# Kernel tuning notes

Hardware: AMD Instinct MI355X
Metric: run time of the kernel (lower is better)

The kernel has to match this reference:

```python
import jax, jax.numpy as jnp
import numpy as np

H = 2048       # hidden_size
E = 8          # num_experts
K = 2          # top_k
I = 16         # expert bottleneck (intermediate_size)


def setup_inputs() -> dict:
    key = jax.random.key(0)
    k1, k2, k3, k4 = jax.random.split(key, 4)
    B, T = 2, 4096
    x = jax.random.normal(k1, (B, T, H), dtype=jnp.float32)
    # nn.Linear weight layout is (out, in); init scale ~ 1/sqrt(fan_in)
    router_w = jax.random.normal(k2, (E, H), dtype=jnp.float32) / np.sqrt(H)
    down_w = jax.random.normal(k3, (E, I, H), dtype=jnp.float32) / np.sqrt(H)
    up_w = jax.random.normal(k4, (E, H, I), dtype=jnp.float32) / np.sqrt(I)
    return {"x": x, "router_w": router_w, "down_w": down_w, "up_w": up_w}


def reference(x, router_w, down_w, up_w):
    # router
    logits = jnp.einsum('bth,eh->bte', x, router_w)        # [B,T,E]
    weights = jax.nn.softmax(logits, axis=-1)
    top_w, top_idx = jax.lax.top_k(weights, K)             # [B,T,K]
    # gate[b,t,e] = softmax weight if e in top-k else 0 (top-k of softmax
    # values are distinct a.s., so masking == scatter of top_w)
    topk_mask = jnp.sum(jax.nn.one_hot(top_idx, E, dtype=x.dtype), axis=-2)  # [B,T,E]
    gate = weights * topk_mask                              # [B,T,E]
    # dense expert compute on all tokens (matches original's redundant compute)
    h = jnp.einsum('bth,eih->beti', x, down_w)             # [B,E,T,I]
    a = jax.nn.silu(h)
    expert_out = jnp.einsum('beti,ehi->beth', a, up_w)     # [B,E,T,H]
    # masked combine
    out = jnp.einsum('beth,bte->bth', expert_out, gate)    # [B,T,H]
    return out
```

## Files before the change

kernel.cpp:

```cpp
#include <hip/hip_runtime.h>
#include <math.h>

#define HDIM 2048
#define NEXP 8
#define IDIM 16
#define N_EI 128
#define TB   16

typedef __attribute__((ext_vector_type(8))) short bf16x8;
typedef __attribute__((ext_vector_type(4))) float f32x4;

static __device__ __forceinline__ short f2bf(float f) {
    union { float f; unsigned u; } v; v.f = f;
    unsigned r = v.u + 0x7fffu + ((v.u >> 16) & 1u);
    return (short)(r >> 16);
}

__global__ __launch_bounds__(256) void prep_kernel(
    const float* __restrict__ x, const float* __restrict__ rw,
    const float* __restrict__ dw, const float* __restrict__ uw,
    float* __restrict__ gate_ws, short* __restrict__ b1p, short* __restrict__ b2p,
    int T, int routerBlocks)
{
    const int bid = blockIdx.x;
    if (bid < routerBlocks) {
        const int wave = threadIdx.x >> 6, lane = threadIdx.x & 63;
        const int t = bid * 4 + wave;
        if (t >= T) return;
        const float* __restrict__ xr = x + (size_t)t * HDIM;
        float4 xv[8];
        #pragma unroll
        for (int j = 0; j < 8; ++j) xv[j] = *(const float4*)(xr + j * 256 + lane * 4);
        float logit[NEXP];
        #pragma unroll
        for (int e = 0; e < NEXP; ++e) {
            const float* __restrict__ wr = rw + (size_t)e * HDIM;
            float acc = 0.f;
            #pragma unroll
            for (int j = 0; j < 8; ++j) {
                float4 wv = *(const float4*)(wr + j * 256 + lane * 4);
                acc += xv[j].x * wv.x + xv[j].y * wv.y + xv[j].z * wv.z + xv[j].w * wv.w;
            }
            #pragma unroll
            for (int s = 1; s < 64; s <<= 1) acc += __shfl_xor(acc, s);
            logit[e] = acc;
        }
        if (lane == 0) {
            float m = logit[0];
            #pragma unroll
            for (int e = 1; e < NEXP; ++e) m = fmaxf(m, logit[e]);
            float w[NEXP], ssum = 0.f;
            #pragma unroll
            for (int e = 0; e < NEXP; ++e) { w[e] = expf(logit[e] - m); ssum += w[e]; }
            const float inv = 1.f / ssum;
            #pragma unroll
            for (int e = 0; e < NEXP; ++e) w[e] *= inv;
            int i1 = 0; float w1 = w[0];
            #pragma unroll
            for (int e = 1; e < NEXP; ++e) if (w[e] > w1) { w1 = w[e]; i1 = e; }
            int i2 = -1; float w2 = -1.f;
            #pragma unroll
            for (int e = 0; e < NEXP; ++e) if (e != i1 && w[e] > w2) { w2 = w[e]; i2 = e; }
            #pragma unroll
            for (int e = 0; e < NEXP; ++e)
                gate_ws[(size_t)t * NEXP + e] = (e == i1) ? w1 : ((e == i2) ? w2 : 0.f);
        }
    } else {
        const int id = (bid - routerBlocks) * 256 + threadIdx.x;
        float4 v0, v1;
        short* dst;
        if (id < 32768) {
            const int kb = id >> 7, n = id & 127;
            const float* __restrict__ src = dw + (size_t)n * HDIM + kb * 8;
            v0 = *(const float4*)(src);
            v1 = *(const float4*)(src + 4);
            dst = b1p + (size_t)id * 8;
        } else {
            const int id2 = id - 32768;
            const int k2b = id2 >> 11, h = id2 & 2047;
            const int e = k2b >> 1, i0 = (k2b & 1) * 8;
            const float* __restrict__ src = uw + ((size_t)e * HDIM + h) * IDIM + i0;
            v0 = *(const float4*)(src);
            v1 = *(const float4*)(src + 4);
            dst = b2p + (size_t)id2 * 8;
        }
        bf16x8 p;
        p[0] = f2bf(v0.x); p[1] = f2bf(v0.y); p[2] = f2bf(v0.z); p[3] = f2bf(v0.w);
        p[4] = f2bf(v1.x); p[5] = f2bf(v1.y); p[6] = f2bf(v1.z); p[7] = f2bf(v1.w);
        *(bf16x8*)dst = p;
    }
}

__global__ __launch_bounds__(512) void moe_mfma_kernel(
    const float* __restrict__ x, const float* __restrict__ gate_ws,
    const short* __restrict__ b1p, const short* __restrict__ b2p,
    float* __restrict__ out, int T)
{
    __shared__ float h_part[TB][132];
    __shared__ short a_s[TB][136];
    __shared__ float gate_s[TB][NEXP];

    const int tid = threadIdx.x;
    const int w = tid >> 6, l = tid & 63;
    const int c = l & 15;
    const int kblk = l >> 4;
    const int t0 = blockIdx.x * TB;

    if (tid < TB * NEXP)
        gate_s[tid >> 3][tid & 7] = gate_ws[(size_t)(t0 + (tid >> 3)) * NEXP + (tid & 7)];
    __syncthreads();

    const int nq = w & 3, kh = w >> 2;
    const int n0 = nq * 32;
    f32x4 acc0 = {0.f, 0.f, 0.f, 0.f}, acc1 = {0.f, 0.f, 0.f, 0.f};
    const float* __restrict__ xrow = x + (size_t)(t0 + c) * HDIM;

    for (int s = 0; s < 32; ++s) {
        const int k0 = kh * 1024 + s * 32;
        const int ka = k0 + kblk * 8;
        float4 a0 = *(const float4*)(xrow + ka);
        float4 a1 = *(const float4*)(xrow + ka + 4);
        bf16x8 xf;
        xf[0] = f2bf(a0.x); xf[1] = f2bf(a0.y); xf[2] = f2bf(a0.z); xf[3] = f2bf(a0.w);
        xf[4] = f2bf(a1.x); xf[5] = f2bf(a1.y); xf[6] = f2bf(a1.z); xf[7] = f2bf(a1.w);
        const short* __restrict__ bbase = b1p + ((size_t)(k0 >> 3) + kblk) * 1024;
        bf16x8 wf0 = *(const bf16x8*)(bbase + (n0 + c) * 8);
        bf16x8 wf1 = *(const bf16x8*)(bbase + (n0 + 16 + c) * 8);
        acc0 = __builtin_amdgcn_mfma_f32_16x16x32_bf16(wf0, xf, acc0, 0, 0, 0);
        acc1 = __builtin_amdgcn_mfma_f32_16x16x32_bf16(wf1, xf, acc1, 0, 0, 0);
    }

    if (kh == 1) {
        *(f32x4*)&h_part[c][n0 + kblk * 4]      = acc0;
        *(f32x4*)&h_part[c][n0 + 16 + kblk * 4] = acc1;
    }
    __syncthreads();
    if (kh == 0) {
        const int e0 = nq * 2, e1 = nq * 2 + 1;
        const f32x4 hp0 = *(const f32x4*)&h_part[c][n0 + kblk * 4];
        const f32x4 hp1 = *(const f32x4*)&h_part[c][n0 + 16 + kblk * 4];
        const float g0 = gate_s[c][e0], g1 = gate_s[c][e1];
        short r0[4], r1[4];
        #pragma unroll
        for (int r = 0; r < 4; ++r) {
            const float h0v = acc0[r] + hp0[r];
            const float h1v = acc1[r] + hp1[r];
            r0[r] = f2bf(h0v / (1.f + expf(-h0v)) * g0);
            r1[r] = f2bf(h1v / (1.f + expf(-h1v)) * g1);
        }
        *(uint2*)&a_s[c][n0 + kblk * 4]      = make_uint2(((unsigned short)r0[0]) | ((unsigned)(unsigned short)r0[1] << 16),
                                                          ((unsigned short)r0[2]) | ((unsigned)(unsigned short)r0[3] << 16));
        *(uint2*)&a_s[c][n0 + 16 + kblk * 4] = make_uint2(((unsigned short)r1[0]) | ((unsigned)(unsigned short)r1[1] << 16),
                                                          ((unsigned short)r1[2]) | ((unsigned)(unsigned short)r1[3] << 16));
    }
    __syncthreads();

    const int h0 = w * 256;
    f32x4 acc[16];
    #pragma unroll
    for (int f = 0; f < 16; ++f) acc[f] = (f32x4){0.f, 0.f, 0.f, 0.f};

    for (int s = 0; s < 4; ++s) {
        bf16x8 af = *(const bf16x8*)(&a_s[c][s * 32 + kblk * 8]);
        const short* __restrict__ bbase = b2p + ((size_t)(s * 4) + kblk) * 16384;
        #pragma unroll
        for (int f = 0; f < 16; ++f) {
            bf16x8 wfr = *(const bf16x8*)(bbase + (size_t)(h0 + f * 16 + c) * 8);
            acc[f] = __builtin_amdgcn_mfma_f32_16x16x32_bf16(wfr, af, acc[f], 0, 0, 0);
        }
    }
    float* __restrict__ orow = out + (size_t)(t0 + c) * HDIM;
    #pragma unroll
    for (int f = 0; f < 16; ++f) {
        __builtin_nontemporal_store(acc[f], (f32x4*)(orow + h0 + f * 16 + kblk * 4));
    }
}

extern "C" void kernel_launch(void* const* d_in, const int* in_sizes, int n_in,
                              void* d_out, int out_size, void* d_ws, size_t ws_size,
                              hipStream_t stream) {
    const float* x  = (const float*)d_in[0];
    const float* rw = (const float*)d_in[1];
    const float* dw = (const float*)d_in[2];
    const float* uw = (const float*)d_in[3];
    float* out = (float*)d_out;
    const int T = in_sizes[0] / HDIM;

    float* gate_ws = (float*)d_ws;
    short* b1p = (short*)((char*)d_ws + (size_t)T * NEXP * 4);
    short* b2p = (short*)((char*)d_ws + (size_t)T * NEXP * 4 + 524288);

    const int routerBlocks = T / 4;
    prep_kernel<<<routerBlocks + 256, 256, 0, stream>>>(x, rw, dw, uw,
                                                        gate_ws, b1p, b2p, T, routerBlocks);
    moe_mfma_kernel<<<T / TB, 512, 0, stream>>>(x, gate_ws, b1p, b2p, out, T);
}
```

Baseline: 180.4 us.

## Double token tile, pre-convert x to bf16, batch router shuffle reductions

Raises the token tile per block from 16 to 32, so each loaded weight fragment feeds two MFMAs in both the down and up projections, which halves weight traffic per token. When the workspace is large enough, the prep kernel also writes a bf16 copy of x so the main kernel reads half the bytes and skips per-element conversion, at the cost of an extra full pass over x. The router's cross-lane reductions are interleaved across all experts for more instruction-level parallelism. Output stores switch from nontemporal to normal stores, and the doubled accumulators raise register pressure with half as many blocks.

Result: faster. 172.5 us (-4.4%).

```diff
diff --git a/kernel.cpp b/kernel.cpp
--- a/kernel.cpp
+++ b/kernel.cpp
@@ -5,7 +5,7 @@
 #define NEXP 8
 #define IDIM 16
 #define N_EI 128
-#define TB   16
+#define TB   32
 
 typedef __attribute__((ext_vector_type(8))) short bf16x8;
 typedef __attribute__((ext_vector_type(4))) float f32x4;
@@ -20,18 +20,17 @@
     const float* __restrict__ x, const float* __restrict__ rw,
     const float* __restrict__ dw, const float* __restrict__ uw,
     float* __restrict__ gate_ws, short* __restrict__ b1p, short* __restrict__ b2p,
-    int T, int routerBlocks)
+    short* __restrict__ x_bf, int T, int routerBlocks)
 {
     const int bid = blockIdx.x;
     if (bid < routerBlocks) {
         const int wave = threadIdx.x >> 6, lane = threadIdx.x & 63;
         const int t = bid * 4 + wave;
-        if (t >= T) return;
         const float* __restrict__ xr = x + (size_t)t * HDIM;
         float4 xv[8];
         #pragma unroll
         for (int j = 0; j < 8; ++j) xv[j] = *(const float4*)(xr + j * 256 + lane * 4);
-        float logit[NEXP];
+        float accv[NEXP];
         #pragma unroll
         for (int e = 0; e < NEXP; ++e) {
             const float* __restrict__ wr = rw + (size_t)e * HDIM;
@@ -41,17 +40,20 @@
                 float4 wv = *(const float4*)(wr + j * 256 + lane * 4);
                 acc += xv[j].x * wv.x + xv[j].y * wv.y + xv[j].z * wv.z + xv[j].w * wv.w;
             }
-            #pragma unroll
-            for (int s = 1; s < 64; s <<= 1) acc += __shfl_xor(acc, s);
-            logit[e] = acc;
+            accv[e] = acc;
+        }
+        #pragma unroll
+        for (int s = 1; s < 64; s <<= 1) {
+            #pragma unroll
+            for (int e = 0; e < NEXP; ++e) accv[e] += __shfl_xor(accv[e], s);
         }
         if (lane == 0) {
-            float m = logit[0];
-            #pragma unroll
-            for (int e = 1; e < NEXP; ++e) m = fmaxf(m, logit[e]);
+            float m = accv[0];
+            #pragma unroll
+            for (int e = 1; e < NEXP; ++e) m = fmaxf(m, accv[e]);
             float w[NEXP], ssum = 0.f;
             #pragma unroll
-            for (int e = 0; e < NEXP; ++e) { w[e] = expf(logit[e] - m); ssum += w[e]; }
+            for (int e = 0; e < NEXP; ++e) { w[e] = expf(accv[e] - m); ssum += w[e]; }
             const float inv = 1.f / ssum;
             #pragma unroll
             for (int e = 0; e < NEXP; ++e) w[e] *= inv;
@@ -65,7 +67,7 @@
             for (int e = 0; e < NEXP; ++e)
                 gate_ws[(size_t)t * NEXP + e] = (e == i1) ? w1 : ((e == i2) ? w2 : 0.f);
         }
-    } else {
+    } else if (bid < routerBlocks + 256) {
         const int id = (bid - routerBlocks) * 256 + threadIdx.x;
         float4 v0, v1;
         short* dst;
@@ -88,11 +90,28 @@
         p[0] = f2bf(v0.x); p[1] = f2bf(v0.y); p[2] = f2bf(v0.z); p[3] = f2bf(v0.w);
         p[4] = f2bf(v1.x); p[5] = f2bf(v1.y); p[6] = f2bf(v1.z); p[7] = f2bf(v1.w);
         *(bf16x8*)dst = p;
-    }
-}
-
+    } else {
+        const size_t gid = (size_t)(bid - routerBlocks - 256) * 256 + threadIdx.x;
+        const size_t base = gid * 16;
+        const float* __restrict__ src = x + base;
+        float4 a = *(const float4*)(src);
+        float4 b = *(const float4*)(src + 4);
+        float4 c = *(const float4*)(src + 8);
+        float4 d = *(const float4*)(src + 12);
+        bf16x8 p0, p1;
+        p0[0] = f2bf(a.x); p0[1] = f2bf(a.y); p0[2] = f2bf(a.z); p0[3] = f2bf(a.w);
+        p0[4] = f2bf(b.x); p0[5] = f2bf(b.y); p0[6] = f2bf(b.z); p0[7] = f2bf(b.w);
+        p1[0] = f2bf(c.x); p1[1] = f2bf(c.y); p1[2] = f2bf(c.z); p1[3] = f2bf(c.w);
+        p1[4] = f2bf(d.x); p1[5] = f2bf(d.y); p1[6] = f2bf(d.z); p1[7] = f2bf(d.w);
+        *(bf16x8*)(x_bf + base) = p0;
+        *(bf16x8*)(x_bf + base + 8) = p1;
+    }
+}
+
+template<bool XBF>
 __global__ __launch_bounds__(512) void moe_mfma_kernel(
-    const float* __restrict__ x, const float* __restrict__ gate_ws,
+    const float* __restrict__ x, const short* __restrict__ x_bf,
+    const float* __restrict__ gate_ws,
     const short* __restrict__ b1p, const short* __restrict__ b2p,
     float* __restrict__ out, int T)
 {
@@ -112,67 +131,98 @@
 
     const int nq = w & 3, kh = w >> 2;
     const int n0 = nq * 32;
-    f32x4 acc0 = {0.f, 0.f, 0.f, 0.f}, acc1 = {0.f, 0.f, 0.f, 0.f};
-    const float* __restrict__ xrow = x + (size_t)(t0 + c) * HDIM;
+    f32x4 acc00 = {0,0,0,0}, acc01 = {0,0,0,0}, acc10 = {0,0,0,0}, acc11 = {0,0,0,0};
+
+    const float* __restrict__ xr0 = x + (size_t)(t0 + c) * HDIM;
+    const float* __restrict__ xr1 = x + (size_t)(t0 + 16 + c) * HDIM;
+    const short* __restrict__ xb0 = x_bf + (size_t)(t0 + c) * HDIM;
+    const short* __restrict__ xb1 = x_bf + (size_t)(t0 + 16 + c) * HDIM;
 
     for (int s = 0; s < 32; ++s) {
         const int k0 = kh * 1024 + s * 32;
         const int ka = k0 + kblk * 8;
-        float4 a0 = *(const float4*)(xrow + ka);
-        float4 a1 = *(const float4*)(xrow + ka + 4);
-        bf16x8 xf;
-        xf[0] = f2bf(a0.x); xf[1] = f2bf(a0.y); xf[2] = f2bf(a0.z); xf[3] = f2bf(a0.w);
-        xf[4] = f2bf(a1.x); xf[5] = f2bf(a1.y); xf[6] = f2bf(a1.z); xf[7] = f2bf(a1.w);
+        bf16x8 xf0, xf1;
+        if (XBF) {
+            xf0 = *(const bf16x8*)(xb0 + ka);
+            xf1 = *(const bf16x8*)(xb1 + ka);
+        } else {
+            float4 a0 = *(const float4*)(xr0 + ka);
+            float4 a1 = *(const float4*)(xr0 + ka + 4);
+            float4 b0 = *(const float4*)(xr1 + ka);
+            float4 b1 = *(const float4*)(xr1 + ka + 4);
+            xf0[0]=f2bf(a0.x); xf0[1]=f2bf(a0.y); xf0[2]=f2bf(a0.z); xf0[3]=f2bf(a0.w);
+            xf0[4]=f2bf(a1.x); xf0[5]=f2bf(a1.y); xf0[6]=f2bf(a1.z); xf0[7]=f2bf(a1.w);
+            xf1[0]=f2bf(b0.x); xf1[1]=f2bf(b0.y); xf1[2]=f2bf(b0.z); xf1[3]=f2bf(b0.w);
+            xf1[4]=f2bf(b1.x); xf1[5]=f2bf(b1.y); xf1[6]=f2bf(b1.z); xf1[7]=f2bf(b1.w);
+        }
         const short* __restrict__ bbase = b1p + ((size_t)(k0 >> 3) + kblk) * 1024;
         bf16x8 wf0 = *(const bf16x8*)(bbase + (n0 + c) * 8);
         bf16x8 wf1 = *(const bf16x8*)(bbase + (n0 + 16 + c) * 8);
-        acc0 = __builtin_amdgcn_mfma_f32_16x16x32_bf16(wf0, xf, acc0, 0, 0, 0);
-        acc1 = __builtin_amdgcn_mfma_f32_16x16x32_bf16(wf1, xf, acc1, 0, 0, 0);
+        acc00 = __builtin_amdgcn_mfma_f32_16x16x32_bf16(wf0, xf0, acc00, 0, 0, 0);
+        acc01 = __builtin_amdgcn_mfma_f32_16x16x32_bf16(wf0, xf1, acc01, 0, 0, 0);
+        acc10 = __builtin_amdgcn_mfma_f32_16x16x32_bf16(wf1, xf0, acc10, 0, 0, 0);
+        acc11 = __builtin_amdgcn_mfma_f32_16x16x32_bf16(wf1, xf1, acc11, 0, 0, 0);
     }
 
     if (kh == 1) {
-        *(f32x4*)&h_part[c][n0 + kblk * 4]      = acc0;
-        *(f32x4*)&h_part[c][n0 + 16 + kblk * 4] = acc1;
+        *(f32x4*)&h_part[c][n0 + kblk * 4]           = acc00;
+        *(f32x4*)&h_part[16 + c][n0 + kblk * 4]      = acc01;
+        *(f32x4*)&h_part[c][n0 + 16 + kblk * 4]      = acc10;
+        *(f32x4*)&h_part[16 + c][n0 + 16 + kblk * 4] = acc11;
     }
     __syncthreads();
     if (kh == 0) {
         const int e0 = nq * 2, e1 = nq * 2 + 1;
-        const f32x4 hp0 = *(const f32x4*)&h_part[c][n0 + kblk * 4];
-        const f32x4 hp1 = *(const f32x4*)&h_part[c][n0 + 16 + kblk * 4];
-        const float g0 = gate_s[c][e0], g1 = gate_s[c][e1];
-        short r0[4], r1[4];
-        #pragma unroll
-        for (int r = 0; r < 4; ++r) {
-            const float h0v = acc0[r] + hp0[r];
-            const float h1v = acc1[r] + hp1[r];
-            r0[r] = f2bf(h0v / (1.f + expf(-h0v)) * g0);
-            r1[r] = f2bf(h1v / (1.f + expf(-h1v)) * g1);
-        }
-        *(uint2*)&a_s[c][n0 + kblk * 4]      = make_uint2(((unsigned short)r0[0]) | ((unsigned)(unsigned short)r0[1] << 16),
-                                                          ((unsigned short)r0[2]) | ((unsigned)(unsigned short)r0[3] << 16));
-        *(uint2*)&a_s[c][n0 + 16 + kblk * 4] = make_uint2(((unsigned short)r1[0]) | ((unsigned)(unsigned short)r1[1] << 16),
-                                                          ((unsigned short)r1[2]) | ((unsigned)(unsigned short)r1[3] << 16));
+        #pragma unroll
+        for (int tf = 0; tf < 2; ++tf) {
+            const int trow = tf * 16 + c;
+            const f32x4 pa = *(const f32x4*)&h_part[trow][n0 + kblk * 4];
+            const f32x4 pb = *(const f32x4*)&h_part[trow][n0 + 16 + kblk * 4];
+            const f32x4 da = tf ? acc01 : acc00;
+            const f32x4 db = tf ? acc11 : acc10;
+            const float g0 = gate_s[trow][e0], g1 = gate_s[trow][e1];
+            short r0[4], r1[4];
+            #pragma unroll
+            for (int r = 0; r < 4; ++r) {
+                const float h0v = da[r] + pa[r];
+                const float h1v = db[r] + pb[r];
+                r0[r] = f2bf(h0v / (1.f + expf(-h0v)) * g0);
+                r1[r] = f2bf(h1v / (1.f + expf(-h1v)) * g1);
+            }
+            *(uint2*)&a_s[trow][n0 + kblk * 4] =
+                make_uint2(((unsigned short)r0[0]) | ((unsigned)(unsigned short)r0[1] << 16),
+                           ((unsigned short)r0[2]) | ((unsigned)(unsigned short)r0[3] << 16));
+            *(uint2*)&a_s[trow][n0 + 16 + kblk * 4] =
+                make_uint2(((unsigned short)r1[0]) | ((unsigned)(unsigned short)r1[1] << 16),
+                           ((unsigned short)r1[2]) | ((unsigned)(unsigned short)r1[3] << 16));
+        }
     }
     __syncthreads();
 
     const int h0 = w * 256;
-    f32x4 acc[16];
+    f32x4 acc[2][16];
     #pragma unroll
-    for (int f = 0; f < 16; ++f) acc[f] = (f32x4){0.f, 0.f, 0.f, 0.f};
+    for (int tf = 0; tf < 2; ++tf)
+        #pragma unroll
+        for (int f = 0; f < 16; ++f) acc[tf][f] = (f32x4){0,0,0,0};
 
     for (int s = 0; s < 4; ++s) {
-        bf16x8 af = *(const bf16x8*)(&a_s[c][s * 32 + kblk * 8]);
+        bf16x8 af0 = *(const bf16x8*)(&a_s[c][s * 32 + kblk * 8]);
+        bf16x8 af1 = *(const bf16x8*)(&a_s[16 + c][s * 32 + kblk * 8]);
         const short* __restrict__ bbase = b2p + ((size_t)(s * 4) + kblk) * 16384;
         #pragma unroll
         for (int f = 0; f < 16; ++f) {
             bf16x8 wfr = *(const bf16x8*)(bbase + (size_t)(h0 + f * 16 + c) * 8);
-            acc[f] = __builtin_amdgcn_mfma_f32_16x16x32_bf16(wfr, af, acc[f], 0, 0, 0);
-        }
-    }
-    float* __restrict__ orow = out + (size_t)(t0 + c) * HDIM;
+            acc[0][f] = __builtin_amdgcn_mfma_f32_16x16x32_bf16(wfr, af0, acc[0][f], 0, 0, 0);
+            acc[1][f] = __builtin_amdgcn_mfma_f32_16x16x32_bf16(wfr, af1, acc[1][f], 0, 0, 0);
+        }
+    }
+    float* __restrict__ o0 = out + (size_t)(t0 + c) * HDIM;
+    float* __restrict__ o1 = out + (size_t)(t0 + 16 + c) * HDIM;
     #pragma unroll
     for (int f = 0; f < 16; ++f) {
-        __builtin_nontemporal_store(acc[f], (f32x4*)(orow + h0 + f * 16 + kblk * 4));
+        *(f32x4*)(o0 + h0 + f * 16 + kblk * 4) = acc[0][f];
+        *(f32x4*)(o1 + h0 + f * 16 + kblk * 4) = acc[1][f];
     }
 }
 
@@ -189,9 +239,18 @@
     float* gate_ws = (float*)d_ws;
     short* b1p = (short*)((char*)d_ws + (size_t)T * NEXP * 4);
     short* b2p = (short*)((char*)d_ws + (size_t)T * NEXP * 4 + 524288);
+    short* x_bf = (short*)((char*)d_ws + (size_t)T * NEXP * 4 + 1048576);
+
+    const size_t ws_needed = (size_t)T * NEXP * 4 + 1048576 + (size_t)T * HDIM * 2;
+    const bool use_xbf = (ws_size >= ws_needed);
 
     const int routerBlocks = T / 4;
-    prep_kernel<<<routerBlocks + 256, 256, 0, stream>>>(x, rw, dw, uw,
-                                                        gate_ws, b1p, b2p, T, routerBlocks);
-    moe_mfma_kernel<<<T / TB, 512, 0, stream>>>(x, gate_ws, b1p, b2p, out, T);
-}
+    const int xcvtBlocks = use_xbf ? (T * HDIM / (256 * 16)) : 0;
+    prep_kernel<<<routerBlocks + 256 + xcvtBlocks, 256, 0, stream>>>(
+        x, rw, dw, uw, gate_ws, b1p, b2p, x_bf, T, routerBlocks);
+
+    if (use_xbf)
+        moe_mfma_kernel<true><<<T / TB, 512, 0, stream>>>(x, x_bf, gate_ws, b1p, b2p, out, T);
+    else
+        moe_mfma_kernel<false><<<T / TB, 512, 0, stream>>>(x, x_bf, gate_ws, b1p, b2p, out, T);
+}
```

## Split fused MoE kernel into down and up kernels with bf16 x cache

Applied to the files above, without the earlier changes.

Splits the single fused kernel into a down-projection kernel that writes gated SiLU activations to global memory and a separate up-projection kernel with a different token/hidden tiling. When workspace allows, the router kernel also writes a bf16 copy of x, which the down kernel reads instead of re-converting fp32. The router's shuffle reductions are batched across experts. This trades an extra launch, extra global round-trips for x_bf and activations, and plain instead of nontemporal output stores for smaller kernels with more independent blocks.

New measurement: 173.1 us. -4.0%, faster.

```diff
diff --git a/kernel.cpp b/kernel.cpp
--- a/kernel.cpp
+++ b/kernel.cpp
@@ -5,7 +5,6 @@
 #define NEXP 8
 #define IDIM 16
 #define N_EI 128
-#define TB   16
 
 typedef __attribute__((ext_vector_type(8))) short bf16x8;
 typedef __attribute__((ext_vector_type(4))) float f32x4;
@@ -20,18 +19,27 @@
     const float* __restrict__ x, const float* __restrict__ rw,
     const float* __restrict__ dw, const float* __restrict__ uw,
     float* __restrict__ gate_ws, short* __restrict__ b1p, short* __restrict__ b2p,
-    int T, int routerBlocks)
+    short* __restrict__ x_bf, int T, int routerBlocks, int doXbf)
 {
     const int bid = blockIdx.x;
     if (bid < routerBlocks) {
         const int wave = threadIdx.x >> 6, lane = threadIdx.x & 63;
         const int t = bid * 4 + wave;
-        if (t >= T) return;
         const float* __restrict__ xr = x + (size_t)t * HDIM;
         float4 xv[8];
         #pragma unroll
         for (int j = 0; j < 8; ++j) xv[j] = *(const float4*)(xr + j * 256 + lane * 4);
-        float logit[NEXP];
+
+        if (doXbf) {
+            #pragma unroll
+            for (int j = 0; j < 8; ++j) {
+                unsigned lo = ((unsigned short)f2bf(xv[j].x)) | ((unsigned)(unsigned short)f2bf(xv[j].y) << 16);
+                unsigned hi = ((unsigned short)f2bf(xv[j].z)) | ((unsigned)(unsigned short)f2bf(xv[j].w) << 16);
+                *(uint2*)(x_bf + (size_t)t * HDIM + j * 256 + lane * 4) = make_uint2(lo, hi);
+            }
+        }
+
+        float accv[NEXP];
         #pragma unroll
         for (int e = 0; e < NEXP; ++e) {
             const float* __restrict__ wr = rw + (size_t)e * HDIM;
@@ -41,17 +49,20 @@
                 float4 wv = *(const float4*)(wr + j * 256 + lane * 4);
                 acc += xv[j].x * wv.x + xv[j].y * wv.y + xv[j].z * wv.z + xv[j].w * wv.w;
             }
-            #pragma unroll
-            for (int s = 1; s < 64; s <<= 1) acc += __shfl_xor(acc, s);
-            logit[e] = acc;
+            accv[e] = acc;
+        }
+        #pragma unroll
+        for (int s = 1; s < 64; s <<= 1) {
+            #pragma unroll
+            for (int e = 0; e < NEXP; ++e) accv[e] += __shfl_xor(accv[e], s);
         }
         if (lane == 0) {
-            float m = logit[0];
-            #pragma unroll
-            for (int e = 1; e < NEXP; ++e) m = fmaxf(m, logit[e]);
+            float m = accv[0];
+            #pragma unroll
+            for (int e = 1; e < NEXP; ++e) m = fmaxf(m, accv[e]);
             float w[NEXP], ssum = 0.f;
             #pragma unroll
-            for (int e = 0; e < NEXP; ++e) { w[e] = expf(logit[e] - m); ssum += w[e]; }
+            for (int e = 0; e < NEXP; ++e) { w[e] = expf(accv[e] - m); ssum += w[e]; }
             const float inv = 1.f / ssum;
             #pragma unroll
             for (int e = 0; e < NEXP; ++e) w[e] *= inv;
@@ -91,38 +102,38 @@
     }
 }
 
-__global__ __launch_bounds__(512) void moe_mfma_kernel(
-    const float* __restrict__ x, const float* __restrict__ gate_ws,
-    const short* __restrict__ b1p, const short* __restrict__ b2p,
-    float* __restrict__ out, int T)
+template<bool XBF>
+__global__ __launch_bounds__(512) void down_kernel(
+    const float* __restrict__ x, const short* __restrict__ x_bf,
+    const float* __restrict__ gate_ws, const short* __restrict__ b1p,
+    short* __restrict__ a_gl, int T)
 {
-    __shared__ float h_part[TB][132];
-    __shared__ short a_s[TB][136];
-    __shared__ float gate_s[TB][NEXP];
+    __shared__ float h_part[16][132];
 
     const int tid = threadIdx.x;
     const int w = tid >> 6, l = tid & 63;
     const int c = l & 15;
     const int kblk = l >> 4;
-    const int t0 = blockIdx.x * TB;
-
-    if (tid < TB * NEXP)
-        gate_s[tid >> 3][tid & 7] = gate_ws[(size_t)(t0 + (tid >> 3)) * NEXP + (tid & 7)];
-    __syncthreads();
-
+    const int t0 = blockIdx.x * 16;
     const int nq = w & 3, kh = w >> 2;
     const int n0 = nq * 32;
-    f32x4 acc0 = {0.f, 0.f, 0.f, 0.f}, acc1 = {0.f, 0.f, 0.f, 0.f};
-    const float* __restrict__ xrow = x + (size_t)(t0 + c) * HDIM;
+
+    f32x4 acc0 = {0,0,0,0}, acc1 = {0,0,0,0};
+    const float* __restrict__ xr = x + (size_t)(t0 + c) * HDIM;
+    const short* __restrict__ xb = x_bf + (size_t)(t0 + c) * HDIM;
 
     for (int s = 0; s < 32; ++s) {
         const int k0 = kh * 1024 + s * 32;
         const int ka = k0 + kblk * 8;
-        float4 a0 = *(const float4*)(xrow + ka);
-        float4 a1 = *(const float4*)(xrow + ka + 4);
         bf16x8 xf;
-        xf[0] = f2bf(a0.x); xf[1] = f2bf(a0.y); xf[2] = f2bf(a0.z); xf[3] = f2bf(a0.w);
-        xf[4] = f2bf(a1.x); xf[5] = f2bf(a1.y); xf[6] = f2bf(a1.z); xf[7] = f2bf(a1.w);
+        if (XBF) {
+            xf = *(const bf16x8*)(xb + ka);
+        } else {
+            float4 a0 = *(const float4*)(xr + ka);
+            float4 a1 = *(const float4*)(xr + ka + 4);
+            xf[0]=f2bf(a0.x); xf[1]=f2bf(a0.y); xf[2]=f2bf(a0.z); xf[3]=f2bf(a0.w);
+            xf[4]=f2bf(a1.x); xf[5]=f2bf(a1.y); xf[6]=f2bf(a1.z); xf[7]=f2bf(a1.w);
+        }
         const short* __restrict__ bbase = b1p + ((size_t)(k0 >> 3) + kblk) * 1024;
         bf16x8 wf0 = *(const bf16x8*)(bbase + (n0 + c) * 8);
         bf16x8 wf1 = *(const bf16x8*)(bbase + (n0 + 16 + c) * 8);
@@ -136,32 +147,49 @@
     }
     __syncthreads();
     if (kh == 0) {
-        const int e0 = nq * 2, e1 = nq * 2 + 1;
-        const f32x4 hp0 = *(const f32x4*)&h_part[c][n0 + kblk * 4];
-        const f32x4 hp1 = *(const f32x4*)&h_part[c][n0 + 16 + kblk * 4];
-        const float g0 = gate_s[c][e0], g1 = gate_s[c][e1];
+        const f32x4 pa = *(const f32x4*)&h_part[c][n0 + kblk * 4];
+        const f32x4 pb = *(const f32x4*)&h_part[c][n0 + 16 + kblk * 4];
+        const float g0 = gate_ws[(size_t)(t0 + c) * NEXP + nq * 2];
+        const float g1 = gate_ws[(size_t)(t0 + c) * NEXP + nq * 2 + 1];
         short r0[4], r1[4];
         #pragma unroll
         for (int r = 0; r < 4; ++r) {
-            const float h0v = acc0[r] + hp0[r];
-            const float h1v = acc1[r] + hp1[r];
+            const float h0v = acc0[r] + pa[r];
+            const float h1v = acc1[r] + pb[r];
             r0[r] = f2bf(h0v / (1.f + expf(-h0v)) * g0);
             r1[r] = f2bf(h1v / (1.f + expf(-h1v)) * g1);
         }
-        *(uint2*)&a_s[c][n0 + kblk * 4]      = make_uint2(((unsigned short)r0[0]) | ((unsigned)(unsigned short)r0[1] << 16),
-                                                          ((unsigned short)r0[2]) | ((unsigned)(unsigned short)r0[3] << 16));
-        *(uint2*)&a_s[c][n0 + 16 + kblk * 4] = make_uint2(((unsigned short)r1[0]) | ((unsigned)(unsigned short)r1[1] << 16),
-                                                          ((unsigned short)r1[2]) | ((unsigned)(unsigned short)r1[3] << 16));
-    }
-    __syncthreads();
-
-    const int h0 = w * 256;
+        short* __restrict__ arow = a_gl + (size_t)(t0 + c) * N_EI;
+        *(uint2*)(arow + n0 + kblk * 4) =
+            make_uint2(((unsigned short)r0[0]) | ((unsigned)(unsigned short)r0[1] << 16),
+                       ((unsigned short)r0[2]) | ((unsigned)(unsigned short)r0[3] << 16));
+        *(uint2*)(arow + n0 + 16 + kblk * 4) =
+            make_uint2(((unsigned short)r1[0]) | ((unsigned)(unsigned short)r1[1] << 16),
+                       ((unsigned short)r1[2]) | ((unsigned)(unsigned short)r1[3] << 16));
+    }
+}
+
+__global__ __launch_bounds__(512) void up_kernel(
+    const short* __restrict__ a_gl, const short* __restrict__ b2p,
+    float* __restrict__ out, int T)
+{
+    const int tid = threadIdx.x;
+    const int w = tid >> 6, l = tid & 63;
+    const int c = l & 15;
+    const int kblk = l >> 4;
+    const int bid = blockIdx.x;
+    const int tgrp = bid >> 1, bh = bid & 1;
+    const int th = w >> 2, hq = w & 3;
+    const int t0 = tgrp * 32 + th * 16;
+    const int h0 = bh * 1024 + hq * 256;
+
     f32x4 acc[16];
     #pragma unroll
-    for (int f = 0; f < 16; ++f) acc[f] = (f32x4){0.f, 0.f, 0.f, 0.f};
-
+    for (int f = 0; f < 16; ++f) acc[f] = (f32x4){0,0,0,0};
+
+    const short* __restrict__ arow = a_gl + (size_t)(t0 + c) * N_EI;
     for (int s = 0; s < 4; ++s) {
-        bf16x8 af = *(const bf16x8*)(&a_s[c][s * 32 + kblk * 8]);
+        bf16x8 af = *(const bf16x8*)(arow + s * 32 + kblk * 8);
         const short* __restrict__ bbase = b2p + ((size_t)(s * 4) + kblk) * 16384;
         #pragma unroll
         for (int f = 0; f < 16; ++f) {
@@ -171,9 +199,8 @@
     }
     float* __restrict__ orow = out + (size_t)(t0 + c) * HDIM;
     #pragma unroll
-    for (int f = 0; f < 16; ++f) {
-        __builtin_nontemporal_store(acc[f], (f32x4*)(orow + h0 + f * 16 + kblk * 4));
-    }
+    for (int f = 0; f < 16; ++f)
+        *(f32x4*)(orow + h0 + f * 16 + kblk * 4) = acc[f];
 }
 
 extern "C" void kernel_launch(void* const* d_in, const int* in_sizes, int n_in,
@@ -186,12 +213,27 @@
     float* out = (float*)d_out;
     const int T = in_sizes[0] / HDIM;
 
-    float* gate_ws = (float*)d_ws;
-    short* b1p = (short*)((char*)d_ws + (size_t)T * NEXP * 4);
-    short* b2p = (short*)((char*)d_ws + (size_t)T * NEXP * 4 + 524288);
+    char* wsb = (char*)d_ws;
+    float* gate_ws = (float*)wsb;
+    short* b1p  = (short*)(wsb + (size_t)T * NEXP * 4);
+    short* b2p  = (short*)(wsb + (size_t)T * NEXP * 4 + 524288);
+    short* x_bf = (short*)(wsb + (size_t)T * NEXP * 4 + 1048576);
+    const size_t xbf_bytes = (size_t)T * HDIM * 2;
+
+    const size_t need_full  = (size_t)T * NEXP * 4 + 1048576 + xbf_bytes + (size_t)T * N_EI * 2;
+    const bool use_xbf = (ws_size >= need_full);
+    short* a_gl = use_xbf
+        ? (short*)(wsb + (size_t)T * NEXP * 4 + 1048576 + xbf_bytes)
+        : (short*)(wsb + (size_t)T * NEXP * 4 + 1048576);
 
     const int routerBlocks = T / 4;
-    prep_kernel<<<routerBlocks + 256, 256, 0, stream>>>(x, rw, dw, uw,
-                                                        gate_ws, b1p, b2p, T, routerBlocks);
-    moe_mfma_kernel<<<T / TB, 512, 0, stream>>>(x, gate_ws, b1p, b2p, out, T);
-}
+    prep_kernel<<<routerBlocks + 256, 256, 0, stream>>>(
+        x, rw, dw, uw, gate_ws, b1p, b2p, x_bf, T, routerBlocks, use_xbf ? 1 : 0);
+
+    if (use_xbf)
+        down_kernel<true><<<T / 16, 512, 0, stream>>>(x, x_bf, gate_ws, b1p, a_gl, T);
+    else
+        down_kernel<false><<<T / 16, 512, 0, stream>>>(x, x_bf, gate_ws, b1p, a_gl, T);
+
+    up_kernel<<<(T / 32) * 2, 512, 0, stream>>>(a_gl, b2p, out, T);
+}
```
